# Kernel tuning notes

Measured on AMD Instinct MI355X. Metric: run time of the kernel, lower is better.

The kernel has to match this reference:

```python
import jax, jax.numpy as jnp
import numpy as np

N = 50000      # nodes
E = 800000     # edges (before self-loops)
DIN = 64
DH = 64
DOUT = 64
G = 500        # graphs in batch
EPS = 1e-5     # BatchNorm eps


def setup_inputs() -> dict:
    key = jax.random.key(0)
    ks = jax.random.split(key, 8)
    x = jax.random.normal(ks[0], (N, DIN), dtype=jnp.float32)
    edge_index = jax.random.randint(ks[1], (2, E), 0, N, dtype=jnp.int32)
    batch = jnp.sort(jax.random.randint(ks[2], (N,), 0, G, dtype=jnp.int32))

    def lin(k, di, do):
        return (jax.random.normal(k, (di, do), dtype=jnp.float32) / np.float32(np.sqrt(di)))

    inp = dict(x=x, edge_index=edge_index, batch=batch)
    dims = [(DIN, DH), (DH, DH), (DH, DOUT)]
    for i, (di, do) in enumerate(dims, start=1):
        inp[f"W{i}"] = lin(ks[2 + i], di, do)
        inp[f"b{i}"] = jnp.zeros((do,), jnp.float32)
        inp[f"gamma{i}"] = jnp.ones((do,), jnp.float32)
        inp[f"beta{i}"] = jnp.zeros((do,), jnp.float32)
    return inp


def _gcn_norm(edge_index, n_nodes):
    # add self loops, compute symmetric normalization deg^-1/2 * deg^-1/2
    loop = jnp.arange(n_nodes, dtype=edge_index.dtype)
    src = jnp.concatenate([edge_index[0], loop])
    dst = jnp.concatenate([edge_index[1], loop])
    deg = jax.ops.segment_sum(jnp.ones_like(dst, dtype=jnp.float32), dst,
                              num_segments=n_nodes)
    dinv = jax.lax.rsqrt(deg)  # deg >= 1 thanks to self-loops
    norm = dinv[src] * dinv[dst]  # [E + N]
    return src, dst, norm


def _gcn_conv(x, src, dst, norm, W, b, n_nodes):
    h = x @ W                               # [N, dout]
    msg = h[src] * norm[:, None]            # gather + scale  [E+N, dout]
    out = jax.ops.segment_sum(msg, dst, num_segments=n_nodes)  # scatter-add
    return out + b


def _batchnorm(x, gamma, beta):
    mean = jnp.mean(x, axis=0)
    var = jnp.mean(jnp.square(x - mean), axis=0)  # biased, as in torch training BN
    return gamma * (x - mean) * jax.lax.rsqrt(var + EPS) + beta


def reference(x, edge_index, batch, W1, b1, gamma1, beta1,
              W2, b2, gamma2, beta2, W3, b3, gamma3, beta3):
    src, dst, norm = _gcn_norm(edge_index, N)
    layers = [(W1, b1, gamma1, beta1), (W2, b2, gamma2, beta2),
              (W3, b3, gamma3, beta3)]
    h = x
    for i, (W, b, g, be) in enumerate(layers):
        h = _gcn_conv(h, src, dst, norm, W, b, N)
        h = _batchnorm(h, g, be)
        if i < len(layers) - 1:
            h = jax.nn.relu(h)  # dropout is identity in eval / reference
    # global mean pool over graphs
    sums = jax.ops.segment_sum(h, batch, num_segments=G)          # [G, DOUT]
    cnts = jax.ops.segment_sum(jnp.ones((N,), jnp.float32), batch,
                               num_segments=G)
    return sums / jnp.maximum(cnts, 1.0)[:, None]
```

## Files before the change

### kernel.cpp

```cpp
#include <hip/hip_runtime.h>
#include <hip/hip_fp16.h>

#define BN_EPS 1e-5f
#define CCH 4096
#define NSLICE 32


__device__ inline __half2 u2h(unsigned u) {
    union { unsigned u; __half2 h; } x; x.u = u; return x.h;
}
__device__ inline unsigned h2u(__half2 h) {
    union { unsigned u; __half2 h; } x; x.h = h; return x.u;
}

__device__ inline unsigned pack_f16x2(float a, float b) {
    return h2u(__floats2half2_rn(a, b));
}


__global__ __launch_bounds__(256) void coarse_count(const int* __restrict__ dst,
                                                    int* __restrict__ ccnt, int E) {
    __shared__ int h[256];
    int t = threadIdx.x;
    h[t] = 0;
    __syncthreads();
    int e0 = blockIdx.x * CCH;
#pragma unroll
    for (int k = 0; k < CCH / 256; ++k) {
        int e = e0 + k * 256 + t;
        if (e < E) atomicAdd(&h[dst[e] >> 8], 1);
    }
    __syncthreads();
    if (h[t]) atomicAdd(&ccnt[t], h[t]);
}

__global__ __launch_bounds__(256) void cscan(const int* __restrict__ ccnt,
                                             int* __restrict__ cboff,
                                             int* __restrict__ gcur,
                                             int* __restrict__ rp,
                                             float* __restrict__ cnt_g,
                                             float* __restrict__ out,
                                             int NBC, int n, int E, int G) {
    __shared__ int s[256];
    int t = threadIdx.x;
    int v = (t < NBC) ? ccnt[t] : 0;
    s[t] = v;
    __syncthreads();
    for (int off = 1; off < 256; off <<= 1) {
        int u = (t >= off) ? s[t - off] : 0;
        __syncthreads();
        s[t] += u;
        __syncthreads();
    }
    int ex = s[t] - v;
    if (t < NBC) { cboff[t] = ex; gcur[t] = ex; }
    if (t == 0) { cboff[NBC] = E; rp[n] = E; }
    for (int i = t; i < G; i += 256) cnt_g[i] = 0.f;
    int tot = G * 64;
    for (int i = t; i < tot; i += 256) out[i] = 0.f;
}

__global__ __launch_bounds__(256) void cscatter(const int* __restrict__ src,
                                                const int* __restrict__ dst,
                                                int* __restrict__ gcur,
                                                unsigned* __restrict__ tmp, int E) {
    __shared__ int lcnt[256];
    int t = threadIdx.x;
    int e0 = blockIdx.x * CCH;
    lcnt[t] = 0;
    __syncthreads();
#pragma unroll
    for (int k = 0; k < CCH / 256; ++k) {
        int e = e0 + k * 256 + t;
        if (e < E) atomicAdd(&lcnt[dst[e] >> 8], 1);
    }
    __syncthreads();
    int c = lcnt[t];
    __syncthreads();
    if (c > 0) lcnt[t] = atomicAdd(&gcur[t], c);
    __syncthreads();
#pragma unroll
    for (int k = 0; k < CCH / 256; ++k) {
        int e = e0 + k * 256 + t;
        if (e < E) {
            int d = dst[e];
            int pos = atomicAdd(&lcnt[d >> 8], 1);
            tmp[pos] = ((unsigned)src[e] << 8) | (unsigned)(d & 255);
        }
    }
}


#define OUT_CAP 8192

__global__ __launch_bounds__(256) void build_csr(const unsigned* __restrict__ tmp,
                                                 const int* __restrict__ cboff,
                                                 int* __restrict__ rp,
                                                 unsigned short* __restrict__ col,
                                                 float* __restrict__ dinv,
                                                 const int* __restrict__ batch,
                                                 float* __restrict__ cnt_g,
                                                 int n, int G) {
    __shared__ int hist[256];
    __shared__ int sc[256];
    __shared__ unsigned short outw[OUT_CAP];
    __shared__ int h[512];
    int b = blockIdx.x;
    int t = threadIdx.x;
    int beg = cboff[b], end = cboff[b + 1];
    int m = end - beg;
    hist[t] = 0;
    __syncthreads();
    for (int e = beg + t; e < end; e += 256) atomicAdd(&hist[tmp[e] & 255u], 1);
    __syncthreads();
    int v = hist[t];
    sc[t] = v;
    __syncthreads();
    for (int off = 1; off < 256; off <<= 1) {
        int u = (t >= off) ? sc[t - off] : 0;
        __syncthreads();
        sc[t] += u;
        __syncthreads();
    }
    int excl = sc[t] - v;
    int node = b * 256 + t;
    if (node < n) {
        dinv[node] = rsqrtf(1.0f + (float)v);
        rp[node] = beg + excl;
    }
    hist[t] = excl;
    __syncthreads();
    if (m <= OUT_CAP) {
        for (int e = beg + t; e < end; e += 256) {
            unsigned p = tmp[e];
            int pos = atomicAdd(&hist[p & 255u], 1);
            outw[pos] = (unsigned short)(p >> 8);
        }
        __syncthreads();
        for (int i = t; i < m; i += 256) col[beg + i] = outw[i];
    } else {
        for (int e = beg + t; e < end; e += 256) {
            unsigned p = tmp[e];
            int pos = atomicAdd(&hist[p & 255u], 1);
            col[beg + pos] = (unsigned short)(p >> 8);
        }
    }
    if (G <= 512) {
        __syncthreads();
        for (int i = t; i < 512; i += 256) h[i] = 0;
        __syncthreads();
        for (int i = b * 256 + t; i < n; i += gridDim.x * 256)
            atomicAdd(&h[batch[i]], 1);
        __syncthreads();
        for (int i = t; i < G; i += 256)
            if (h[i]) atomicAdd(&cnt_g[i], (float)h[i]);
    } else {
        for (int i = b * 256 + t; i < n; i += gridDim.x * 256)
            atomicAdd(&cnt_g[batch[i]], 1.0f);
    }
}


#define SXS 68

__global__ __launch_bounds__(256) void gemm64_v2(const float* __restrict__ X,
                                                 const float* __restrict__ W,
                                                 const float* __restrict__ dinv,
                                                 const float* __restrict__ part,
                                                 const float* __restrict__ gamma,
                                                 const float* __restrict__ beta,
                                                 int has_bn, float inv_n,
                                                 unsigned* __restrict__ Hs, int n) {
    __shared__ float sX[64 * SXS];
    __shared__ float sW[64 * SXS];
    __shared__ float s_scsh[128];
    int t = threadIdx.x;
    int c4 = t & 15;
    int base = blockIdx.x * 64;

    if (has_bn) {
        if (t < 128) {
            float s = 0.f;
#pragma unroll
            for (int k = 0; k < NSLICE; ++k) s += part[k * 128 + t];
            s_scsh[t] = s;
        }
        __syncthreads();
        if (t < 64) {
            float mean = s_scsh[t] * inv_n;
            float var = s_scsh[64 + t] * inv_n - mean * mean;
            float sc = gamma[t] * rsqrtf(var + BN_EPS);
            s_scsh[t] = sc;
            s_scsh[64 + t] = beta[t] - mean * sc;
        }
        __syncthreads();
    }

    {
        const float4* W4 = (const float4*)W;
#pragma unroll
        for (int it = 0; it < 4; ++it) {
            int idx = it * 256 + t;
            int r = idx >> 4;
            float4 v = W4[r * 16 + c4];
            *(float4*)&sW[r * SXS + c4 * 4] = v;
        }
    }
    {
        const float4* X4 = (const float4*)X;
        float4 sc4, sh4;
        if (has_bn) {
            sc4 = *(const float4*)&s_scsh[c4 * 4];
            sh4 = *(const float4*)&s_scsh[64 + c4 * 4];
        }
#pragma unroll
        for (int it = 0; it < 4; ++it) {
            int idx = it * 256 + t;
            int r = idx >> 4;
            int grow = base + r;
            float4 v = make_float4(0.f, 0.f, 0.f, 0.f);
            if (grow < n) v = X4[(size_t)grow * 16 + c4];
            if (has_bn) {
                v.x = fmaxf(fmaf(v.x, sc4.x, sh4.x), 0.f);
                v.y = fmaxf(fmaf(v.y, sc4.y, sh4.y), 0.f);
                v.z = fmaxf(fmaf(v.z, sc4.z, sh4.z), 0.f);
                v.w = fmaxf(fmaf(v.w, sc4.w, sh4.w), 0.f);
            }
            *(float4*)&sX[r * SXS + c4 * 4] = v;
        }
    }
    __syncthreads();

    int rgrp = t >> 4;
    float4 acc[4];
#pragma unroll
    for (int ri = 0; ri < 4; ++ri) acc[ri] = make_float4(0.f, 0.f, 0.f, 0.f);

#pragma unroll 4
    for (int k4 = 0; k4 < 16; ++k4) {
        float4 xv[4], wv[4];
#pragma unroll
        for (int ri = 0; ri < 4; ++ri)
            xv[ri] = *(const float4*)&sX[(rgrp + 16 * ri) * SXS + k4 * 4];
#pragma unroll
        for (int kk = 0; kk < 4; ++kk)
            wv[kk] = *(const float4*)&sW[(k4 * 4 + kk) * SXS + c4 * 4];
#pragma unroll
        for (int ri = 0; ri < 4; ++ri) {
            acc[ri].x = fmaf(xv[ri].x, wv[0].x, acc[ri].x);
            acc[ri].y = fmaf(xv[ri].x, wv[0].y, acc[ri].y);
            acc[ri].z = fmaf(xv[ri].x, wv[0].z, acc[ri].z);
            acc[ri].w = fmaf(xv[ri].x, wv[0].w, acc[ri].w);
            acc[ri].x = fmaf(xv[ri].y, wv[1].x, acc[ri].x);
            acc[ri].y = fmaf(xv[ri].y, wv[1].y, acc[ri].y);
            acc[ri].z = fmaf(xv[ri].y, wv[1].z, acc[ri].z);
            acc[ri].w = fmaf(xv[ri].y, wv[1].w, acc[ri].w);
            acc[ri].x = fmaf(xv[ri].z, wv[2].x, acc[ri].x);
            acc[ri].y = fmaf(xv[ri].z, wv[2].y, acc[ri].y);
            acc[ri].z = fmaf(xv[ri].z, wv[2].z, acc[ri].z);
            acc[ri].w = fmaf(xv[ri].z, wv[2].w, acc[ri].w);
            acc[ri].x = fmaf(xv[ri].w, wv[3].x, acc[ri].x);
            acc[ri].y = fmaf(xv[ri].w, wv[3].y, acc[ri].y);
            acc[ri].z = fmaf(xv[ri].w, wv[3].z, acc[ri].z);
            acc[ri].w = fmaf(xv[ri].w, wv[3].w, acc[ri].w);
        }
    }

#pragma unroll
    for (int ri = 0; ri < 4; ++ri) {
        int row = base + rgrp + 16 * ri;
        if (row < n) {
            float dv = dinv[row];
            uint2 o2;
            o2.x = pack_f16x2(acc[ri].x * dv, acc[ri].y * dv);
            o2.y = pack_f16x2(acc[ri].z * dv, acc[ri].w * dv);
            ((uint2*)Hs)[(size_t)row * 16 + c4] = o2;
        }
    }
}


__global__ __launch_bounds__(256) void agg(const uint4* __restrict__ Hs4,
                                           const int* __restrict__ rp,
                                           const unsigned short* __restrict__ col,
                                           const float* __restrict__ dinv,
                                           float* __restrict__ Y,
                                           float* __restrict__ part, int n) {
    __shared__ float sS[4][64];
    __shared__ float sQ[4][64];
    int t = threadIdx.x;
    int w = t >> 6;
    int lane = t & 63;
    int g = lane >> 3;
    int c = lane & 7;
    int d = blockIdx.x * 4 + w;
    bool valid = d < n;
    int dc = valid ? d : 0;
    __half2 a0 = u2h(0u), a1 = u2h(0u), a2 = u2h(0u), a3 = u2h(0u);
    int beg = valid ? rp[dc] : 0;
    int end = valid ? rp[dc + 1] : 0;
    for (int b = beg; b < end; b += 64) {
        int m = min(64, end - b);
        int myidx = (lane < m) ? (int)col[b + lane] : 0;
        int jj = 0;
        for (; jj + 15 < m; jj += 16) {
            int s0 = __shfl(myidx, jj + g, 64);
            int s1 = __shfl(myidx, jj + 8 + g, 64);
            uint4 v0 = Hs4[(size_t)s0 * 8 + c];
            uint4 v1 = Hs4[(size_t)s1 * 8 + c];
            a0 = __hadd2(a0, u2h(v0.x)); a1 = __hadd2(a1, u2h(v0.y));
            a2 = __hadd2(a2, u2h(v0.z)); a3 = __hadd2(a3, u2h(v0.w));
            a0 = __hadd2(a0, u2h(v1.x)); a1 = __hadd2(a1, u2h(v1.y));
            a2 = __hadd2(a2, u2h(v1.z)); a3 = __hadd2(a3, u2h(v1.w));
        }
        for (; jj < m; jj += 8) {
            int e = jj + g;
            int s0 = __shfl(myidx, e, 64);
            if (e < m) {
                uint4 v = Hs4[(size_t)s0 * 8 + c];
                a0 = __hadd2(a0, u2h(v.x)); a1 = __hadd2(a1, u2h(v.y));
                a2 = __hadd2(a2, u2h(v.z)); a3 = __hadd2(a3, u2h(v.w));
            }
        }
    }
#pragma unroll
    for (int mask = 8; mask <= 32; mask <<= 1) {
        a0 = __hadd2(a0, u2h((unsigned)__shfl_xor((int)h2u(a0), mask, 64)));
        a1 = __hadd2(a1, u2h((unsigned)__shfl_xor((int)h2u(a1), mask, 64)));
        a2 = __hadd2(a2, u2h((unsigned)__shfl_xor((int)h2u(a2), mask, 64)));
        a3 = __hadd2(a3, u2h((unsigned)__shfl_xor((int)h2u(a3), mask, 64)));
    }
    if (g == 0) {
        float2 f0 = __half22float2(a0), f1 = __half22float2(a1);
        float2 f2 = __half22float2(a2), f3 = __half22float2(a3);
        float y0 = f0.x, y1 = f0.y, y2 = f1.x, y3 = f1.y;
        float y4 = f2.x, y5 = f2.y, y6 = f3.x, y7 = f3.y;
        if (valid) {
            uint4 hv = Hs4[(size_t)dc * 8 + c];
            float2 h0 = __half22float2(u2h(hv.x)), h1 = __half22float2(u2h(hv.y));
            float2 h2v = __half22float2(u2h(hv.z)), h3 = __half22float2(u2h(hv.w));
            float dv = dinv[dc];
            y0 = (y0 + h0.x) * dv; y1 = (y1 + h0.y) * dv;
            y2 = (y2 + h1.x) * dv; y3 = (y3 + h1.y) * dv;
            y4 = (y4 + h2v.x) * dv; y5 = (y5 + h2v.y) * dv;
            y6 = (y6 + h3.x) * dv; y7 = (y7 + h3.y) * dv;
            *(float4*)&Y[(size_t)dc * 64 + c * 8]     = make_float4(y0, y1, y2, y3);
            *(float4*)&Y[(size_t)dc * 64 + c * 8 + 4] = make_float4(y4, y5, y6, y7);
        } else {
            y0 = y1 = y2 = y3 = y4 = y5 = y6 = y7 = 0.f;
        }
        *(float4*)&sS[w][c * 8]     = make_float4(y0, y1, y2, y3);
        *(float4*)&sS[w][c * 8 + 4] = make_float4(y4, y5, y6, y7);
        *(float4*)&sQ[w][c * 8]     = make_float4(y0 * y0, y1 * y1, y2 * y2, y3 * y3);
        *(float4*)&sQ[w][c * 8 + 4] = make_float4(y4 * y4, y5 * y5, y6 * y6, y7 * y7);
    }
    __syncthreads();
    if (t < 64) {
        float s = sS[0][t] + sS[1][t] + sS[2][t] + sS[3][t];
        float qq = sQ[0][t] + sQ[1][t] + sQ[2][t] + sQ[3][t];
        float* dst = part + (size_t)(blockIdx.x & (NSLICE - 1)) * 128;
        atomicAdd(&dst[t], s);
        atomicAdd(&dst[64 + t], qq);
    }
}

__global__ __launch_bounds__(256) void agg_pool(const uint4* __restrict__ Hs4,
                                                const int* __restrict__ rp,
                                                const unsigned short* __restrict__ col,
                                                const float* __restrict__ dinv,
                                                const int* __restrict__ batch,
                                                float* __restrict__ out,
                                                float* __restrict__ part, int n) {
    __shared__ float sS[4][64];
    __shared__ float sQ[4][64];
    __shared__ int sG[4];
    int t = threadIdx.x;
    int w = t >> 6;
    int lane = t & 63;
    int g = lane >> 3;
    int c = lane & 7;
    int d = blockIdx.x * 4 + w;
    bool valid = d < n;
    int dc = valid ? d : 0;
    __half2 a0 = u2h(0u), a1 = u2h(0u), a2 = u2h(0u), a3 = u2h(0u);
    int beg = valid ? rp[dc] : 0;
    int end = valid ? rp[dc + 1] : 0;
    for (int b = beg; b < end; b += 64) {
        int m = min(64, end - b);
        int myidx = (lane < m) ? (int)col[b + lane] : 0;
        int jj = 0;
        for (; jj + 15 < m; jj += 16) {
            int s0 = __shfl(myidx, jj + g, 64);
            int s1 = __shfl(myidx, jj + 8 + g, 64);
            uint4 v0 = Hs4[(size_t)s0 * 8 + c];
            uint4 v1 = Hs4[(size_t)s1 * 8 + c];
            a0 = __hadd2(a0, u2h(v0.x)); a1 = __hadd2(a1, u2h(v0.y));
            a2 = __hadd2(a2, u2h(v0.z)); a3 = __hadd2(a3, u2h(v0.w));
            a0 = __hadd2(a0, u2h(v1.x)); a1 = __hadd2(a1, u2h(v1.y));
            a2 = __hadd2(a2, u2h(v1.z)); a3 = __hadd2(a3, u2h(v1.w));
        }
        for (; jj < m; jj += 8) {
            int e = jj + g;
            int s0 = __shfl(myidx, e, 64);
            if (e < m) {
                uint4 v = Hs4[(size_t)s0 * 8 + c];
                a0 = __hadd2(a0, u2h(v.x)); a1 = __hadd2(a1, u2h(v.y));
                a2 = __hadd2(a2, u2h(v.z)); a3 = __hadd2(a3, u2h(v.w));
            }
        }
    }
#pragma unroll
    for (int mask = 8; mask <= 32; mask <<= 1) {
        a0 = __hadd2(a0, u2h((unsigned)__shfl_xor((int)h2u(a0), mask, 64)));
        a1 = __hadd2(a1, u2h((unsigned)__shfl_xor((int)h2u(a1), mask, 64)));
        a2 = __hadd2(a2, u2h((unsigned)__shfl_xor((int)h2u(a2), mask, 64)));
        a3 = __hadd2(a3, u2h((unsigned)__shfl_xor((int)h2u(a3), mask, 64)));
    }
    if (g == 0) {
        float2 f0 = __half22float2(a0), f1 = __half22float2(a1);
        float2 f2 = __half22float2(a2), f3 = __half22float2(a3);
        float y0 = f0.x, y1 = f0.y, y2 = f1.x, y3 = f1.y;
        float y4 = f2.x, y5 = f2.y, y6 = f3.x, y7 = f3.y;
        if (valid) {
            uint4 hv = Hs4[(size_t)dc * 8 + c];
            float2 h0 = __half22float2(u2h(hv.x)), h1 = __half22float2(u2h(hv.y));
            float2 h2v = __half22float2(u2h(hv.z)), h3 = __half22float2(u2h(hv.w));
            float dv = dinv[dc];
            y0 = (y0 + h0.x) * dv; y1 = (y1 + h0.y) * dv;
            y2 = (y2 + h1.x) * dv; y3 = (y3 + h1.y) * dv;
            y4 = (y4 + h2v.x) * dv; y5 = (y5 + h2v.y) * dv;
            y6 = (y6 + h3.x) * dv; y7 = (y7 + h3.y) * dv;
        } else {
            y0 = y1 = y2 = y3 = y4 = y5 = y6 = y7 = 0.f;
        }
        *(float4*)&sS[w][c * 8]     = make_float4(y0, y1, y2, y3);
        *(float4*)&sS[w][c * 8 + 4] = make_float4(y4, y5, y6, y7);
        *(float4*)&sQ[w][c * 8]     = make_float4(y0 * y0, y1 * y1, y2 * y2, y3 * y3);
        *(float4*)&sQ[w][c * 8 + 4] = make_float4(y4 * y4, y5 * y5, y6 * y6, y7 * y7);
        if (lane == 0) sG[w] = valid ? batch[dc] : -1;
    }
    __syncthreads();
    if (t < 64) {
        float s = sS[0][t] + sS[1][t] + sS[2][t] + sS[3][t];
        float qq = sQ[0][t] + sQ[1][t] + sQ[2][t] + sQ[3][t];
        float* dst = part + (size_t)(blockIdx.x & (NSLICE - 1)) * 128;
        atomicAdd(&dst[t], s);
        atomicAdd(&dst[64 + t], qq);
        int g0 = sG[0], g1 = sG[1], g2 = sG[2], g3 = sG[3];
        if (g0 >= 0 && g0 == g1 && g0 == g2 && g0 == g3) {
            atomicAdd(&out[(size_t)g0 * 64 + t], s);
        } else {
            if (g0 >= 0) atomicAdd(&out[(size_t)g0 * 64 + t], sS[0][t]);
            if (g1 >= 0) atomicAdd(&out[(size_t)g1 * 64 + t], sS[1][t]);
            if (g2 >= 0) atomicAdd(&out[(size_t)g2 * 64 + t], sS[2][t]);
            if (g3 >= 0) atomicAdd(&out[(size_t)g3 * 64 + t], sS[3][t]);
        }
    }
}


__global__ __launch_bounds__(256) void pool_div(float* __restrict__ out,
                                                const float* __restrict__ cnt,
                                                const float* __restrict__ part,
                                                const float* __restrict__ gamma,
                                                const float* __restrict__ beta,
                                                int G, float inv_n) {
    __shared__ float s_scsh[128];
    int t = threadIdx.x;
    if (t < 128) {
        float s = 0.f;
#pragma unroll
        for (int k = 0; k < NSLICE; ++k) s += part[k * 128 + t];
        s_scsh[t] = s;
    }
    __syncthreads();
    if (t < 64) {
        float mean = s_scsh[t] * inv_n;
        float var = s_scsh[64 + t] * inv_n - mean * mean;
        float sc = gamma[t] * rsqrtf(var + BN_EPS);
        s_scsh[t] = sc;
        s_scsh[64 + t] = beta[t] - mean * sc;
    }
    __syncthreads();
    int idx = blockIdx.x * 256 + t;
    if (idx >= G * 64) return;
    int j = idx & 63, g = idx >> 6;
    float c = cnt[g];
    out[idx] = (c > 0.5f) ? fmaf(s_scsh[j], out[idx] / c, s_scsh[64 + j]) : 0.f;
}


extern "C" void kernel_launch(void* const* d_in, const int* in_sizes, int n_in,
                              void* d_out, int out_size, void* d_ws, size_t ws_size,
                              hipStream_t stream) {
    const float* x     = (const float*)d_in[0];
    const int*   ei    = (const int*)d_in[1];
    const int*   batch = (const int*)d_in[2];
    const float* Wl[3] = {(const float*)d_in[3], (const float*)d_in[7], (const float*)d_in[11]};
    const float* gl[3] = {(const float*)d_in[5], (const float*)d_in[9], (const float*)d_in[13]};
    const float* bl[3] = {(const float*)d_in[6], (const float*)d_in[10], (const float*)d_in[14]};
    float* out = (float*)d_out;

    int E = in_sizes[1] / 2;
    int n = in_sizes[0] / 64;
    int G = out_size / 64;
    const int* src = ei;
    const int* dst = ei + E;
    int NBC = (n + 255) / 256;
    float inv_n = 1.0f / (float)n;

    char* ws = (char*)d_ws;
    size_t off = 0;
    auto carve = [&](size_t bytes) {
        void* p = ws + off;
        off += (bytes + 255) & ~(size_t)255;
        return p;
    };
    float*          part  = (float*)carve(3 * NSLICE * 128 * 4);
    int*            ccnt  = (int*)carve(256 * 4);
    float*          dinv  = (float*)carve((size_t)n * 4);
    float*          cnt_g = (float*)carve((size_t)G * 4);
    unsigned*       Hs    = (unsigned*)carve((size_t)n * 32 * 4);
    float*          Ybuf  = (float*)carve((size_t)n * 64 * 4);
    int*            cboff = (int*)carve(257 * 4);
    int*            gcur  = (int*)carve(256 * 4);
    int*            rp    = (int*)carve(((size_t)n + 1) * 4);
    unsigned*       tmp   = (unsigned*)carve((size_t)E * 4);
    unsigned short* col   = (unsigned short*)carve((size_t)E * 2);

    int pgrid = (E + CCH - 1) / CCH;

    hipMemsetAsync(part, 0, 3 * NSLICE * 128 * 4 + 256 * 4, stream);
    coarse_count<<<pgrid, 256, 0, stream>>>(dst, ccnt, E);
    cscan<<<1, 256, 0, stream>>>(ccnt, cboff, gcur, rp, cnt_g, out, NBC, n, E, G);
    cscatter<<<pgrid, 256, 0, stream>>>(src, dst, gcur, tmp, E);
    build_csr<<<NBC, 256, 0, stream>>>(tmp, cboff, rp, col, dinv, batch, cnt_g, n, G);

    int gemm_grid = (n + 63) / 64;
    int agg_grid = (n + 3) / 4;

    const float* cur = x;
    for (int l = 0; l < 3; ++l) {
        float* part_l = part + (size_t)l * NSLICE * 128;
        const float* part_prev = (l > 0) ? part + (size_t)(l - 1) * NSLICE * 128 : part;
        gemm64_v2<<<gemm_grid, 256, 0, stream>>>(cur, Wl[l], dinv, part_prev,
                                                 l > 0 ? gl[l - 1] : gl[0],
                                                 l > 0 ? bl[l - 1] : bl[0],
                                                 l > 0 ? 1 : 0, inv_n, Hs, n);
        if (l < 2) {
            agg<<<agg_grid, 256, 0, stream>>>((const uint4*)Hs, rp, col, dinv,
                                              Ybuf, part_l, n);
        } else {
            agg_pool<<<agg_grid, 256, 0, stream>>>((const uint4*)Hs, rp, col, dinv,
                                                   batch, out, part_l, n);
        }
        cur = Ybuf;
    }

    pool_div<<<(G * 64 + 255) / 256, 256, 0, stream>>>(out, cnt_g,
                                                       part + 2 * NSLICE * 128,
                                                       gl[2], bl[2], G, inv_n);
}
```

Before: 253.8 us.

## Fuse whole GCN pipeline into one persistent cooperative kernel with grid syncs

Replaces the sequence of separate launches (memset, CSR build stages, per-layer GEMM and aggregation, pooling) with a single cooperative persistent kernel. Stages are separated by grid-wide barriers and each stage loops over virtual blocks. This removes per-launch overhead and inter-kernel gaps. In exchange, occupancy is capped by the union shared-memory footprint (the GEMM tiles) for every phase, grid syncs add their own latency, and the original multi-kernel path is kept as a fallback.

```diff
diff --git a/kernel.cpp b/kernel.cpp
--- a/kernel.cpp
+++ b/kernel.cpp
@@ -1,9 +1,14 @@
 #include <hip/hip_runtime.h>
 #include <hip/hip_fp16.h>
+#include <hip/hip_cooperative_groups.h>
+
+namespace cg = cooperative_groups;
 
 #define BN_EPS 1e-5f
 #define CCH 4096
 #define NSLICE 32
+#define OUT_CAP 8192
+#define SXS 68
 
 
 __device__ inline __half2 u2h(unsigned u) {
@@ -15,6 +20,403 @@
 
 __device__ inline unsigned pack_f16x2(float a, float b) {
     return h2u(__floats2half2_rn(a, b));
+}
+
+
+struct FParams {
+    const float* x;
+    const int* src;
+    const int* dst;
+    const int* batch;
+    const float* W0; const float* W1; const float* W2;
+    const float* g0; const float* g1; const float* g2;
+    const float* b0; const float* b1; const float* b2;
+    float* out;
+    float* part;
+    int* ccnt;
+    float* dinv;
+    float* cnt_g;
+    unsigned* Hs;
+    float* Ybuf;
+    int* cboff;
+    int* gcur;
+    int* rp;
+    unsigned* tmp;
+    unsigned short* col;
+    int n, E, G, NBC, PG, GEMM_VB, AGG_VB;
+    float inv_n;
+};
+
+union __align__(16) FSm {
+    int h256[256];
+    struct { int hist[256]; int sc[256]; unsigned short outw[OUT_CAP]; int gh[512]; } csr;
+    struct { float sX[64 * SXS]; float sW[64 * SXS]; float scsh[128]; } gm;
+    struct { float sS[4][64]; float sQ[4][64]; int sG[4]; } ag;
+};
+
+__global__ __launch_bounds__(256) void fused_all(FParams p) {
+    cg::grid_group gg = cg::this_grid();
+    __shared__ FSm sm;
+    const int t = threadIdx.x;
+    const int nb = gridDim.x;
+    const int bi = blockIdx.x;
+
+    {
+        int tid = bi * 256 + t;
+        int stride = nb * 256;
+        for (int i = tid; i < 3 * NSLICE * 128; i += stride) p.part[i] = 0.f;
+        if (tid < 256) p.ccnt[tid] = 0;
+        for (int i = tid; i < p.G; i += stride) p.cnt_g[i] = 0.f;
+        for (int i = tid; i < p.G * 64; i += stride) p.out[i] = 0.f;
+    }
+    gg.sync();
+
+    for (int vb = bi; vb < p.PG; vb += nb) {
+        sm.h256[t] = 0;
+        __syncthreads();
+        int e0 = vb * CCH;
+#pragma unroll
+        for (int k = 0; k < CCH / 256; ++k) {
+            int e = e0 + k * 256 + t;
+            if (e < p.E) atomicAdd(&sm.h256[p.dst[e] >> 8], 1);
+        }
+        __syncthreads();
+        if (sm.h256[t]) atomicAdd(&p.ccnt[t], sm.h256[t]);
+        __syncthreads();
+    }
+    gg.sync();
+
+    if (bi == 0) {
+        int v = (t < p.NBC) ? p.ccnt[t] : 0;
+        sm.h256[t] = v;
+        __syncthreads();
+        for (int off = 1; off < 256; off <<= 1) {
+            int u = (t >= off) ? sm.h256[t - off] : 0;
+            __syncthreads();
+            sm.h256[t] += u;
+            __syncthreads();
+        }
+        int ex = sm.h256[t] - v;
+        if (t < p.NBC) { p.cboff[t] = ex; p.gcur[t] = ex; }
+        if (t == 0) { p.cboff[p.NBC] = p.E; p.rp[p.n] = p.E; }
+    }
+    gg.sync();
+
+    for (int vb = bi; vb < p.PG; vb += nb) {
+        sm.h256[t] = 0;
+        __syncthreads();
+        int e0 = vb * CCH;
+#pragma unroll
+        for (int k = 0; k < CCH / 256; ++k) {
+            int e = e0 + k * 256 + t;
+            if (e < p.E) atomicAdd(&sm.h256[p.dst[e] >> 8], 1);
+        }
+        __syncthreads();
+        int c = sm.h256[t];
+        __syncthreads();
+        if (c > 0) sm.h256[t] = atomicAdd(&p.gcur[t], c);
+        __syncthreads();
+#pragma unroll
+        for (int k = 0; k < CCH / 256; ++k) {
+            int e = e0 + k * 256 + t;
+            if (e < p.E) {
+                int d = p.dst[e];
+                int pos = atomicAdd(&sm.h256[d >> 8], 1);
+                p.tmp[pos] = ((unsigned)p.src[e] << 8) | (unsigned)(d & 255);
+            }
+        }
+        __syncthreads();
+    }
+    gg.sync();
+
+    for (int vb = bi; vb < p.NBC; vb += nb) {
+        int beg = p.cboff[vb], end = p.cboff[vb + 1];
+        int m = end - beg;
+        sm.csr.hist[t] = 0;
+        __syncthreads();
+        for (int e = beg + t; e < end; e += 256) atomicAdd(&sm.csr.hist[p.tmp[e] & 255u], 1);
+        __syncthreads();
+        int v = sm.csr.hist[t];
+        sm.csr.sc[t] = v;
+        __syncthreads();
+        for (int off = 1; off < 256; off <<= 1) {
+            int u = (t >= off) ? sm.csr.sc[t - off] : 0;
+            __syncthreads();
+            sm.csr.sc[t] += u;
+            __syncthreads();
+        }
+        int excl = sm.csr.sc[t] - v;
+        int node = vb * 256 + t;
+        if (node < p.n) {
+            p.dinv[node] = rsqrtf(1.0f + (float)v);
+            p.rp[node] = beg + excl;
+        }
+        sm.csr.hist[t] = excl;
+        __syncthreads();
+        if (m <= OUT_CAP) {
+            for (int e = beg + t; e < end; e += 256) {
+                unsigned pk = p.tmp[e];
+                int pos = atomicAdd(&sm.csr.hist[pk & 255u], 1);
+                sm.csr.outw[pos] = (unsigned short)(pk >> 8);
+            }
+            __syncthreads();
+            for (int i = t; i < m; i += 256) p.col[beg + i] = sm.csr.outw[i];
+        } else {
+            for (int e = beg + t; e < end; e += 256) {
+                unsigned pk = p.tmp[e];
+                int pos = atomicAdd(&sm.csr.hist[pk & 255u], 1);
+                p.col[beg + pos] = (unsigned short)(pk >> 8);
+            }
+        }
+        if (p.G <= 512) {
+            __syncthreads();
+            for (int i = t; i < 512; i += 256) sm.csr.gh[i] = 0;
+            __syncthreads();
+            for (int i = vb * 256 + t; i < p.n; i += p.NBC * 256)
+                atomicAdd(&sm.csr.gh[p.batch[i]], 1);
+            __syncthreads();
+            for (int i = t; i < p.G; i += 256)
+                if (sm.csr.gh[i]) atomicAdd(&p.cnt_g[i], (float)sm.csr.gh[i]);
+        } else {
+            for (int i = vb * 256 + t; i < p.n; i += p.NBC * 256)
+                atomicAdd(&p.cnt_g[p.batch[i]], 1.0f);
+        }
+        __syncthreads();
+    }
+    gg.sync();
+
+    const float* cur = p.x;
+    const int c4 = t & 15;
+    const int rgrp = t >> 4;
+#pragma unroll 1
+    for (int l = 0; l < 3; ++l) {
+        const float* Wc = (l == 0) ? p.W0 : (l == 1) ? p.W1 : p.W2;
+        const float* gprev = (l == 1) ? p.g0 : p.g1;
+        const float* bprev = (l == 1) ? p.b0 : p.b1;
+        float* part_l = p.part + (size_t)l * NSLICE * 128;
+        const float* part_prev = p.part + (size_t)(l > 0 ? l - 1 : 0) * NSLICE * 128;
+        int has_bn = (l > 0);
+
+        float4 sc4 = make_float4(0.f, 0.f, 0.f, 0.f), sh4 = make_float4(0.f, 0.f, 0.f, 0.f);
+        if (has_bn) {
+            if (t < 128) {
+                float s = 0.f;
+#pragma unroll
+                for (int k = 0; k < NSLICE; ++k) s += part_prev[k * 128 + t];
+                sm.gm.scsh[t] = s;
+            }
+            __syncthreads();
+            if (t < 64) {
+                float mean = sm.gm.scsh[t] * p.inv_n;
+                float var = sm.gm.scsh[64 + t] * p.inv_n - mean * mean;
+                float sc = gprev[t] * rsqrtf(var + BN_EPS);
+                sm.gm.scsh[t] = sc;
+                sm.gm.scsh[64 + t] = bprev[t] - mean * sc;
+            }
+            __syncthreads();
+            sc4 = *(const float4*)&sm.gm.scsh[c4 * 4];
+            sh4 = *(const float4*)&sm.gm.scsh[64 + c4 * 4];
+            __syncthreads();
+        }
+
+        {
+            const float4* W4 = (const float4*)Wc;
+            const float4* X4 = (const float4*)cur;
+            for (int vb = bi; vb < p.GEMM_VB; vb += nb) {
+                int base = vb * 64;
+#pragma unroll
+                for (int it = 0; it < 4; ++it) {
+                    int idx = it * 256 + t;
+                    int r = idx >> 4;
+                    float4 wv = W4[r * 16 + c4];
+                    *(float4*)&sm.gm.sW[r * SXS + c4 * 4] = wv;
+                }
+#pragma unroll
+                for (int it = 0; it < 4; ++it) {
+                    int idx = it * 256 + t;
+                    int r = idx >> 4;
+                    int grow = base + r;
+                    float4 v = make_float4(0.f, 0.f, 0.f, 0.f);
+                    if (grow < p.n) v = X4[(size_t)grow * 16 + c4];
+                    if (has_bn) {
+                        v.x = fmaxf(fmaf(v.x, sc4.x, sh4.x), 0.f);
+                        v.y = fmaxf(fmaf(v.y, sc4.y, sh4.y), 0.f);
+                        v.z = fmaxf(fmaf(v.z, sc4.z, sh4.z), 0.f);
+                        v.w = fmaxf(fmaf(v.w, sc4.w, sh4.w), 0.f);
+                    }
+                    *(float4*)&sm.gm.sX[r * SXS + c4 * 4] = v;
+                }
+                __syncthreads();
+
+                float4 acc[4];
+#pragma unroll
+                for (int ri = 0; ri < 4; ++ri) acc[ri] = make_float4(0.f, 0.f, 0.f, 0.f);
+#pragma unroll 4
+                for (int k4 = 0; k4 < 16; ++k4) {
+                    float4 xv[4], wv[4];
+#pragma unroll
+                    for (int ri = 0; ri < 4; ++ri)
+                        xv[ri] = *(const float4*)&sm.gm.sX[(rgrp + 16 * ri) * SXS + k4 * 4];
+#pragma unroll
+                    for (int kk = 0; kk < 4; ++kk)
+                        wv[kk] = *(const float4*)&sm.gm.sW[(k4 * 4 + kk) * SXS + c4 * 4];
+#pragma unroll
+                    for (int ri = 0; ri < 4; ++ri) {
+                        acc[ri].x = fmaf(xv[ri].x, wv[0].x, acc[ri].x);
+                        acc[ri].y = fmaf(xv[ri].x, wv[0].y, acc[ri].y);
+                        acc[ri].z = fmaf(xv[ri].x, wv[0].z, acc[ri].z);
+                        acc[ri].w = fmaf(xv[ri].x, wv[0].w, acc[ri].w);
+                        acc[ri].x = fmaf(xv[ri].y, wv[1].x, acc[ri].x);
+                        acc[ri].y = fmaf(xv[ri].y, wv[1].y, acc[ri].y);
+                        acc[ri].z = fmaf(xv[ri].y, wv[1].z, acc[ri].z);
+                        acc[ri].w = fmaf(xv[ri].y, wv[1].w, acc[ri].w);
+                        acc[ri].x = fmaf(xv[ri].z, wv[2].x, acc[ri].x);
+                        acc[ri].y = fmaf(xv[ri].z, wv[2].y, acc[ri].y);
+                        acc[ri].z = fmaf(xv[ri].z, wv[2].z, acc[ri].z);
+                        acc[ri].w = fmaf(xv[ri].z, wv[2].w, acc[ri].w);
+                        acc[ri].x = fmaf(xv[ri].w, wv[3].x, acc[ri].x);
+                        acc[ri].y = fmaf(xv[ri].w, wv[3].y, acc[ri].y);
+                        acc[ri].z = fmaf(xv[ri].w, wv[3].z, acc[ri].z);
+                        acc[ri].w = fmaf(xv[ri].w, wv[3].w, acc[ri].w);
+                    }
+                }
+#pragma unroll
+                for (int ri = 0; ri < 4; ++ri) {
+                    int row = base + rgrp + 16 * ri;
+                    if (row < p.n) {
+                        float dv = p.dinv[row];
+                        uint2 o2;
+                        o2.x = pack_f16x2(acc[ri].x * dv, acc[ri].y * dv);
+                        o2.y = pack_f16x2(acc[ri].z * dv, acc[ri].w * dv);
+                        ((uint2*)p.Hs)[(size_t)row * 16 + c4] = o2;
+                    }
+                }
+                __syncthreads();
+            }
+        }
+        gg.sync();
+
+        {
+            const uint4* Hs4 = (const uint4*)p.Hs;
+            int w = t >> 6;
+            int lane = t & 63;
+            int gsl = lane >> 3;
+            int cc = lane & 7;
+            for (int vb = bi; vb < p.AGG_VB; vb += nb) {
+                int d = vb * 4 + w;
+                bool valid = d < p.n;
+                int dc = valid ? d : 0;
+                __half2 a0 = u2h(0u), a1 = u2h(0u), a2 = u2h(0u), a3 = u2h(0u);
+                int beg = valid ? p.rp[dc] : 0;
+                int end = valid ? p.rp[dc + 1] : 0;
+                for (int b = beg; b < end; b += 64) {
+                    int m = min(64, end - b);
+                    int myidx = (lane < m) ? (int)p.col[b + lane] : 0;
+                    int jj = 0;
+                    for (; jj + 15 < m; jj += 16) {
+                        int s0 = __shfl(myidx, jj + gsl, 64);
+                        int s1 = __shfl(myidx, jj + 8 + gsl, 64);
+                        uint4 v0 = Hs4[(size_t)s0 * 8 + cc];
+                        uint4 v1 = Hs4[(size_t)s1 * 8 + cc];
+                        a0 = __hadd2(a0, u2h(v0.x)); a1 = __hadd2(a1, u2h(v0.y));
+                        a2 = __hadd2(a2, u2h(v0.z)); a3 = __hadd2(a3, u2h(v0.w));
+                        a0 = __hadd2(a0, u2h(v1.x)); a1 = __hadd2(a1, u2h(v1.y));
+                        a2 = __hadd2(a2, u2h(v1.z)); a3 = __hadd2(a3, u2h(v1.w));
+                    }
+                    for (; jj < m; jj += 8) {
+                        int e = jj + gsl;
+                        int s0 = __shfl(myidx, e, 64);
+                        if (e < m) {
+                            uint4 v = Hs4[(size_t)s0 * 8 + cc];
+                            a0 = __hadd2(a0, u2h(v.x)); a1 = __hadd2(a1, u2h(v.y));
+                            a2 = __hadd2(a2, u2h(v.z)); a3 = __hadd2(a3, u2h(v.w));
+                        }
+                    }
+                }
+#pragma unroll
+                for (int mask = 8; mask <= 32; mask <<= 1) {
+                    a0 = __hadd2(a0, u2h((unsigned)__shfl_xor((int)h2u(a0), mask, 64)));
+                    a1 = __hadd2(a1, u2h((unsigned)__shfl_xor((int)h2u(a1), mask, 64)));
+                    a2 = __hadd2(a2, u2h((unsigned)__shfl_xor((int)h2u(a2), mask, 64)));
+                    a3 = __hadd2(a3, u2h((unsigned)__shfl_xor((int)h2u(a3), mask, 64)));
+                }
+                if (gsl == 0) {
+                    float2 f0 = __half22float2(a0), f1 = __half22float2(a1);
+                    float2 f2 = __half22float2(a2), f3 = __half22float2(a3);
+                    float y0 = f0.x, y1 = f0.y, y2 = f1.x, y3 = f1.y;
+                    float y4 = f2.x, y5 = f2.y, y6 = f3.x, y7 = f3.y;
+                    if (valid) {
+                        uint4 hv = Hs4[(size_t)dc * 8 + cc];
+                        float2 h0 = __half22float2(u2h(hv.x)), h1 = __half22float2(u2h(hv.y));
+                        float2 h2v = __half22float2(u2h(hv.z)), h3 = __half22float2(u2h(hv.w));
+                        float dv = p.dinv[dc];
+                        y0 = (y0 + h0.x) * dv; y1 = (y1 + h0.y) * dv;
+                        y2 = (y2 + h1.x) * dv; y3 = (y3 + h1.y) * dv;
+                        y4 = (y4 + h2v.x) * dv; y5 = (y5 + h2v.y) * dv;
+                        y6 = (y6 + h3.x) * dv; y7 = (y7 + h3.y) * dv;
+                        if (l < 2) {
+                            *(float4*)&p.Ybuf[(size_t)dc * 64 + cc * 8]     = make_float4(y0, y1, y2, y3);
+                            *(float4*)&p.Ybuf[(size_t)dc * 64 + cc * 8 + 4] = make_float4(y4, y5, y6, y7);
+                        }
+                    } else {
+                        y0 = y1 = y2 = y3 = y4 = y5 = y6 = y7 = 0.f;
+                    }
+                    *(float4*)&sm.ag.sS[w][cc * 8]     = make_float4(y0, y1, y2, y3);
+                    *(float4*)&sm.ag.sS[w][cc * 8 + 4] = make_float4(y4, y5, y6, y7);
+                    *(float4*)&sm.ag.sQ[w][cc * 8]     = make_float4(y0 * y0, y1 * y1, y2 * y2, y3 * y3);
+                    *(float4*)&sm.ag.sQ[w][cc * 8 + 4] = make_float4(y4 * y4, y5 * y5, y6 * y6, y7 * y7);
+                    if (l == 2 && lane == 0) sm.ag.sG[w] = valid ? p.batch[dc] : -1;
+                }
+                __syncthreads();
+                if (t < 64) {
+                    float s = sm.ag.sS[0][t] + sm.ag.sS[1][t] + sm.ag.sS[2][t] + sm.ag.sS[3][t];
+                    float qq = sm.ag.sQ[0][t] + sm.ag.sQ[1][t] + sm.ag.sQ[2][t] + sm.ag.sQ[3][t];
+                    float* pdst = part_l + (size_t)(vb & (NSLICE - 1)) * 128;
+                    atomicAdd(&pdst[t], s);
+                    atomicAdd(&pdst[64 + t], qq);
+                    if (l == 2) {
+                        int g0 = sm.ag.sG[0], g1 = sm.ag.sG[1], g2 = sm.ag.sG[2], g3 = sm.ag.sG[3];
+                        if (g0 >= 0 && g0 == g1 && g0 == g2 && g0 == g3) {
+                            atomicAdd(&p.out[(size_t)g0 * 64 + t], s);
+                        } else {
+                            if (g0 >= 0) atomicAdd(&p.out[(size_t)g0 * 64 + t], sm.ag.sS[0][t]);
+                            if (g1 >= 0) atomicAdd(&p.out[(size_t)g1 * 64 + t], sm.ag.sS[1][t]);
+                            if (g2 >= 0) atomicAdd(&p.out[(size_t)g2 * 64 + t], sm.ag.sS[2][t]);
+                            if (g3 >= 0) atomicAdd(&p.out[(size_t)g3 * 64 + t], sm.ag.sS[3][t]);
+                        }
+                    }
+                }
+                __syncthreads();
+            }
+        }
+        gg.sync();
+        cur = p.Ybuf;
+    }
+
+    {
+        const float* part2 = p.part + (size_t)2 * NSLICE * 128;
+        if (t < 128) {
+            float s = 0.f;
+#pragma unroll
+            for (int k = 0; k < NSLICE; ++k) s += part2[k * 128 + t];
+            sm.gm.scsh[t] = s;
+        }
+        __syncthreads();
+        if (t < 64) {
+            float mean = sm.gm.scsh[t] * p.inv_n;
+            float var = sm.gm.scsh[64 + t] * p.inv_n - mean * mean;
+            float sc = p.g2[t] * rsqrtf(var + BN_EPS);
+            sm.gm.scsh[t] = sc;
+            sm.gm.scsh[64 + t] = p.b2[t] - mean * sc;
+        }
+        __syncthreads();
+        int stride = nb * 256;
+        for (int idx = bi * 256 + t; idx < p.G * 64; idx += stride) {
+            int j = idx & 63, g = idx >> 6;
+            float c = p.cnt_g[g];
+            p.out[idx] = (c > 0.5f) ? fmaf(sm.gm.scsh[j], p.out[idx] / c, sm.gm.scsh[64 + j]) : 0.f;
+        }
+    }
 }
 
 
@@ -89,9 +491,6 @@
         }
     }
 }
-
-
-#define OUT_CAP 8192
 
 __global__ __launch_bounds__(256) void build_csr(const unsigned* __restrict__ tmp,
                                                  const int* __restrict__ cboff,
@@ -160,9 +559,6 @@
     }
 }
 
-
-#define SXS 68
-
 __global__ __launch_bounds__(256) void gemm64_v2(const float* __restrict__ X,
                                                  const float* __restrict__ W,
                                                  const float* __restrict__ dinv,
@@ -278,7 +674,6 @@
         }
     }
 }
-
 
 __global__ __launch_bounds__(256) void agg(const uint4* __restrict__ Hs4,
                                            const int* __restrict__ rp,
@@ -458,7 +853,6 @@
     }
 }
 
-
 __global__ __launch_bounds__(256) void pool_div(float* __restrict__ out,
                                                 const float* __restrict__ cnt,
                                                 const float* __restrict__ part,
@@ -529,35 +923,68 @@
     unsigned short* col   = (unsigned short*)carve((size_t)E * 2);
 
     int pgrid = (E + CCH - 1) / CCH;
-
-    hipMemsetAsync(part, 0, 3 * NSLICE * 128 * 4 + 256 * 4, stream);
-    coarse_count<<<pgrid, 256, 0, stream>>>(dst, ccnt, E);
-    cscan<<<1, 256, 0, stream>>>(ccnt, cboff, gcur, rp, cnt_g, out, NBC, n, E, G);
-    cscatter<<<pgrid, 256, 0, stream>>>(src, dst, gcur, tmp, E);
-    build_csr<<<NBC, 256, 0, stream>>>(tmp, cboff, rp, col, dinv, batch, cnt_g, n, G);
-
     int gemm_grid = (n + 63) / 64;
     int agg_grid = (n + 3) / 4;
 
-    const float* cur = x;
-    for (int l = 0; l < 3; ++l) {
-        float* part_l = part + (size_t)l * NSLICE * 128;
-        const float* part_prev = (l > 0) ? part + (size_t)(l - 1) * NSLICE * 128 : part;
-        gemm64_v2<<<gemm_grid, 256, 0, stream>>>(cur, Wl[l], dinv, part_prev,
-                                                 l > 0 ? gl[l - 1] : gl[0],
-                                                 l > 0 ? bl[l - 1] : bl[0],
-                                                 l > 0 ? 1 : 0, inv_n, Hs, n);
-        if (l < 2) {
-            agg<<<agg_grid, 256, 0, stream>>>((const uint4*)Hs, rp, col, dinv,
-                                              Ybuf, part_l, n);
-        } else {
-            agg_pool<<<agg_grid, 256, 0, stream>>>((const uint4*)Hs, rp, col, dinv,
-                                                   batch, out, part_l, n);
-        }
-        cur = Ybuf;
-    }
-
-    pool_div<<<(G * 64 + 255) / 256, 256, 0, stream>>>(out, cnt_g,
-                                                       part + 2 * NSLICE * 128,
-                                                       gl[2], bl[2], G, inv_n);
-}
+    static int coopBlocks = -2;
+    if (coopBlocks == -2) {
+        int perCU = 0;
+        hipError_t oe = hipOccupancyMaxActiveBlocksPerMultiprocessor(&perCU, fused_all, 256, 0);
+        int dev = 0;
+        hipGetDevice(&dev);
+        hipDeviceProp_t prop;
+        hipError_t pe = hipGetDeviceProperties(&prop, dev);
+        if (oe == hipSuccess && pe == hipSuccess && perCU > 0 && prop.cooperativeLaunch)
+            coopBlocks = perCU * prop.multiProcessorCount;
+        else
+            coopBlocks = -1;
+    }
+
+    bool launched = false;
+    if (coopBlocks > 0) {
+        FParams p;
+        p.x = x; p.src = src; p.dst = dst; p.batch = batch;
+        p.W0 = Wl[0]; p.W1 = Wl[1]; p.W2 = Wl[2];
+        p.g0 = gl[0]; p.g1 = gl[1]; p.g2 = gl[2];
+        p.b0 = bl[0]; p.b1 = bl[1]; p.b2 = bl[2];
+        p.out = out; p.part = part; p.ccnt = ccnt; p.dinv = dinv; p.cnt_g = cnt_g;
+        p.Hs = Hs; p.Ybuf = Ybuf; p.cboff = cboff; p.gcur = gcur; p.rp = rp;
+        p.tmp = tmp; p.col = col;
+        p.n = n; p.E = E; p.G = G; p.NBC = NBC; p.PG = pgrid;
+        p.GEMM_VB = gemm_grid; p.AGG_VB = agg_grid; p.inv_n = inv_n;
+        void* args[] = { (void*)&p };
+        hipError_t e = hipLaunchCooperativeKernel(fused_all, dim3(coopBlocks), dim3(256),
+                                                  args, 0, stream);
+        if (e == hipSuccess) launched = true;
+        else coopBlocks = -1;
+    }
+
+    if (!launched) {
+        hipMemsetAsync(part, 0, 3 * NSLICE * 128 * 4 + 256 * 4, stream);
+        coarse_count<<<pgrid, 256, 0, stream>>>(dst, ccnt, E);
+        cscan<<<1, 256, 0, stream>>>(ccnt, cboff, gcur, rp, cnt_g, out, NBC, n, E, G);
+        cscatter<<<pgrid, 256, 0, stream>>>(src, dst, gcur, tmp, E);
+        build_csr<<<NBC, 256, 0, stream>>>(tmp, cboff, rp, col, dinv, batch, cnt_g, n, G);
+
+        const float* cur = x;
+        for (int l = 0; l < 3; ++l) {
+            float* part_l = part + (size_t)l * NSLICE * 128;
+            const float* part_prev = (l > 0) ? part + (size_t)(l - 1) * NSLICE * 128 : part;
+            gemm64_v2<<<gemm_grid, 256, 0, stream>>>(cur, Wl[l], dinv, part_prev,
+                                                     l > 0 ? gl[l - 1] : gl[0],
+                                                     l > 0 ? bl[l - 1] : bl[0],
+                                                     l > 0 ? 1 : 0, inv_n, Hs, n);
+            if (l < 2) {
+                agg<<<agg_grid, 256, 0, stream>>>((const uint4*)Hs, rp, col, dinv,
+                                                  Ybuf, part_l, n);
+            } else {
+                agg_pool<<<agg_grid, 256, 0, stream>>>((const uint4*)Hs, rp, col, dinv,
+                                                       batch, out, part_l, n);
+            }
+            cur = Ybuf;
+        }
+        pool_div<<<(G * 64 + 255) / 256, 256, 0, stream>>>(out, cnt_g,
+                                                           part + 2 * NSLICE * 128,
+                                                           gl[2], bl[2], G, inv_n);
+    }
+}
```

New measurement: 829.6 us. 3.27x slower.
